# Kernel optimization log

Hardware: AMD Instinct MI355X
Metric: run time of the kernel (lower is better)

Reference implementation:

```python
import jax, jax.numpy as jnp
import numpy as np

B, H, W, C = 4, 128, 128, 256
D_MODEL, NH = 512, 8
DH = D_MODEL // NH  # 64


def setup_inputs() -> dict:
    key = jax.random.key(0)
    ks = jax.random.split(key, 5)
    s = lambda fan_in: 1.0 / np.sqrt(fan_in)
    return {
        "x": jax.random.normal(ks[0], (B, H, W, C), jnp.float32),
        "Wq": jax.random.normal(ks[1], (C, D_MODEL), jnp.float32) * s(C),
        "bq": jnp.zeros((D_MODEL,), jnp.float32),
        "Wk": jax.random.normal(ks[2], (C, D_MODEL), jnp.float32) * s(C),
        "bk": jnp.zeros((D_MODEL,), jnp.float32),
        "Wv": jax.random.normal(ks[3], (C, D_MODEL), jnp.float32) * s(C),
        "bv": jnp.zeros((D_MODEL,), jnp.float32),
        "Wo": jax.random.normal(ks[4], (D_MODEL, C), jnp.float32) * s(D_MODEL),
        "bo": jnp.zeros((C,), jnp.float32),
    }


def reference(x, Wq, bq, Wk, bk, Wv, bv, Wo, bo):
    # Axial multi-head attention along axis 1 (H), W axis is batched.
    b, h, w, _ = x.shape
    q = (x @ Wq + bq).reshape(b, h, w, NH, DH) * (DH ** -0.5)
    k = (x @ Wk + bk).reshape(b, h, w, NH, DH)
    v = (x @ Wv + bv).reshape(b, h, w, NH, DH)
    # scores over the H axis: [B, Nh, W, H, H]
    scores = jnp.einsum("bxwnd,bywnd->bnwxy", q, k)
    probs = jax.nn.softmax(scores, axis=-1)
    # [B, H, W, Nh, DH] -> [B, H, W, d_model]
    out = jnp.einsum("bnwxy,bywnd->bxwnd", probs, v).reshape(b, h, w, D_MODEL)
    # Wo projection; original combines to [B,W,H,C] then permutes back to [B,H,W,C],
    # which is equivalent to applying Wo directly here. Dropout is identity at inference.
    return out @ Wo + bo
```

## Files before the change

### kernel.cpp

```cpp
#include <hip/hip_runtime.h>

typedef unsigned short u16;
typedef __attribute__((ext_vector_type(8))) short bf16x8;
typedef __attribute__((ext_vector_type(8))) unsigned short u16x8;
typedef __attribute__((ext_vector_type(4))) unsigned short u16x4;
typedef __attribute__((ext_vector_type(4))) unsigned u32x4;
typedef __attribute__((ext_vector_type(4))) float f32x4;

#define DEVI static __device__ __forceinline__

DEVI u16 f2b(float f) {
  unsigned u = __builtin_bit_cast(unsigned, f);
  return (u16)((u + 0x7FFFu + ((u >> 16) & 1u)) >> 16);
}

DEVI unsigned cvtpk(float a, float b) {
  unsigned r;
  asm("v_cvt_pk_bf16_f32 %0, %1, %2" : "=v"(r) : "v"(a), "v"(b));
  return r;
}


__global__ __launch_bounds__(256) void prep_x2(const float* __restrict__ x, u16* __restrict__ xb2) {
  const int n8 = 65536 * 256 / 8;
  int i = blockIdx.x * blockDim.x + threadIdx.x;
  for (; i < n8; i += gridDim.x * blockDim.x) {
    const float4* p = (const float4*)x + (size_t)i * 2;
    float4 a = p[0], b = p[1];
    u16x8 r;
    r[0] = f2b(a.x); r[1] = f2b(a.y); r[2] = f2b(a.z); r[3] = f2b(a.w);
    r[4] = f2b(b.x); r[5] = f2b(b.y); r[6] = f2b(b.z); r[7] = f2b(b.w);
    const int t = i >> 5, c0 = (i & 31) * 8;
    const int b_ = t >> 14, y = (t >> 7) & 127, w = t & 127;
    *(u16x8*)(xb2 + (((size_t)(b_ * 128 + w) * 128) + y) * 256 + c0) = r;
  }
}

__global__ __launch_bounds__(256) void prep_w(
    const float* __restrict__ Wq, const float* __restrict__ Wk,
    const float* __restrict__ Wv, const float* __restrict__ Wo,
    const float* __restrict__ bq, const float* __restrict__ bk, const float* __restrict__ bv,
    u16* __restrict__ wqkvT, u16* __restrict__ woT, float* __restrict__ bqkv) {
  const int NW1 = 1536 * 256, NW2 = 256 * 512;
  const int total = NW1 + NW2 + 1536;
  int i = blockIdx.x * blockDim.x + threadIdx.x;
  for (; i < total; i += gridDim.x * blockDim.x) {
    if (i < NW1) {
      int nn = i >> 8, kk = i & 255;
      float v;
      if (nn < 512)       v = Wq[kk * 512 + nn] * 0.125f;
      else if (nn < 1024) v = Wk[kk * 512 + (nn - 512)];
      else                v = Wv[kk * 512 + (nn - 1024)];
      wqkvT[i] = f2b(v);
    } else if (i < NW1 + NW2) {
      int j = i - NW1;
      int nn = j >> 9, kk = j & 511;
      woT[j] = f2b(Wo[kk * 256 + nn]);
    } else {
      int j = i - NW1 - NW2;
      bqkv[j] = (j < 512) ? bq[j] * 0.125f : (j < 1024 ? bk[j - 512] : bv[j - 1024]);
    }
  }
}


__global__ __launch_bounds__(256) void qkv_attn(
    const u16* __restrict__ xb2, const u16* __restrict__ wqkvT,
    const float* __restrict__ bqkv, u16* __restrict__ ao) {
  __shared__ u16 smem[24576];
  u16* qld = smem;
  u16* kld = smem + 8192;
  u16* vt  = smem + 16384;

  const int g = blockIdx.x;
  const int n = g & 7, ct = g >> 3;
  const int tid = threadIdx.x, lane = tid & 63, wid = tid >> 6;
  const int hi = lane >> 4, lo = lane & 15;
  const int wr = wid >> 1, wc = wid & 1;

  const u16* Xp = xb2 + (size_t)ct * 32768;
  const u16* Wq = wqkvT + (size_t)(n * 64 + wc * 32) * 256;
  const u16* Wk = Wq + 512 * 256;
  const u16* Wv = Wq + 1024 * 256;

  bf16x8 areg[4][8];
#pragma unroll
  for (int yT = 0; yT < 4; ++yT)
#pragma unroll
    for (int ks = 0; ks < 8; ++ks)
      areg[yT][ks] = *(const bf16x8*)(Xp + (wr * 64 + yT * 16 + lo) * 256 + hi * 8 + ks * 32);

  {
    f32x4 acc[2][4];
#pragma unroll
    for (int dhT = 0; dhT < 2; ++dhT)
#pragma unroll
      for (int yT = 0; yT < 4; ++yT) acc[dhT][yT] = f32x4{0.f, 0.f, 0.f, 0.f};
#pragma unroll
    for (int ks = 0; ks < 8; ++ks) {
      bf16x8 wf0 = *(const bf16x8*)(Wq + (0 * 16 + lo) * 256 + hi * 8 + ks * 32);
      bf16x8 wf1 = *(const bf16x8*)(Wq + (1 * 16 + lo) * 256 + hi * 8 + ks * 32);
#pragma unroll
      for (int yT = 0; yT < 4; ++yT) {
        acc[0][yT] = __builtin_amdgcn_mfma_f32_16x16x32_bf16(wf0, areg[yT][ks], acc[0][yT], 0, 0, 0);
        acc[1][yT] = __builtin_amdgcn_mfma_f32_16x16x32_bf16(wf1, areg[yT][ks], acc[1][yT], 0, 0, 0);
      }
    }
#pragma unroll
    for (int dhT = 0; dhT < 2; ++dhT) {
      const int dh0 = wc * 32 + dhT * 16 + hi * 4;
      float4 bq4 = *(const float4*)&bqkv[n * 64 + dh0];
#pragma unroll
      for (int yT = 0; yT < 4; ++yT) {
        const int y = wr * 64 + yT * 16 + lo;
        u16x4 pk;
        pk[0] = f2b(acc[dhT][yT][0] + bq4.x);
        pk[1] = f2b(acc[dhT][yT][1] + bq4.y);
        pk[2] = f2b(acc[dhT][yT][2] + bq4.z);
        pk[3] = f2b(acc[dhT][yT][3] + bq4.w);
        *(u16x4*)&qld[y * 64 + (((dh0 >> 3) ^ (y & 7)) << 3) + (dh0 & 7)] = pk;
      }
    }
  }

  {
    f32x4 acc[2][4];
#pragma unroll
    for (int dhT = 0; dhT < 2; ++dhT)
#pragma unroll
      for (int yT = 0; yT < 4; ++yT) acc[dhT][yT] = f32x4{0.f, 0.f, 0.f, 0.f};
#pragma unroll
    for (int ks = 0; ks < 8; ++ks) {
      bf16x8 wf0 = *(const bf16x8*)(Wk + (0 * 16 + lo) * 256 + hi * 8 + ks * 32);
      bf16x8 wf1 = *(const bf16x8*)(Wk + (1 * 16 + lo) * 256 + hi * 8 + ks * 32);
#pragma unroll
      for (int yT = 0; yT < 4; ++yT) {
        acc[0][yT] = __builtin_amdgcn_mfma_f32_16x16x32_bf16(wf0, areg[yT][ks], acc[0][yT], 0, 0, 0);
        acc[1][yT] = __builtin_amdgcn_mfma_f32_16x16x32_bf16(wf1, areg[yT][ks], acc[1][yT], 0, 0, 0);
      }
    }
#pragma unroll
    for (int dhT = 0; dhT < 2; ++dhT) {
      const int dh0 = wc * 32 + dhT * 16 + hi * 4;
#pragma unroll
      for (int yT = 0; yT < 4; ++yT) {
        const int y = wr * 64 + yT * 16 + lo;
        u16x4 pk;
        pk[0] = f2b(acc[dhT][yT][0]);
        pk[1] = f2b(acc[dhT][yT][1]);
        pk[2] = f2b(acc[dhT][yT][2]);
        pk[3] = f2b(acc[dhT][yT][3]);
        *(u16x4*)&kld[y * 64 + (((dh0 >> 3) ^ (y & 7)) << 3) + (dh0 & 7)] = pk;
      }
    }
  }

  {
    f32x4 acc[4][2];
#pragma unroll
    for (int yT = 0; yT < 4; ++yT)
#pragma unroll
      for (int dhT = 0; dhT < 2; ++dhT) acc[yT][dhT] = f32x4{0.f, 0.f, 0.f, 0.f};
#pragma unroll
    for (int ks = 0; ks < 8; ++ks) {
      bf16x8 wf0 = *(const bf16x8*)(Wv + (0 * 16 + lo) * 256 + hi * 8 + ks * 32);
      bf16x8 wf1 = *(const bf16x8*)(Wv + (1 * 16 + lo) * 256 + hi * 8 + ks * 32);
#pragma unroll
      for (int yT = 0; yT < 4; ++yT) {
        acc[yT][0] = __builtin_amdgcn_mfma_f32_16x16x32_bf16(areg[yT][ks], wf0, acc[yT][0], 0, 0, 0);
        acc[yT][1] = __builtin_amdgcn_mfma_f32_16x16x32_bf16(areg[yT][ks], wf1, acc[yT][1], 0, 0, 0);
      }
    }
#pragma unroll
    for (int dhT = 0; dhT < 2; ++dhT) {
      const int dh = wc * 32 + dhT * 16 + lo;
      const float bv = bqkv[1024 + n * 64 + dh];
#pragma unroll
      for (int yT = 0; yT < 4; ++yT) {
        const int y0 = wr * 64 + yT * 16 + hi * 4;
        const int cch = y0 >> 3;
        u16x4 pk;
        pk[0] = f2b(acc[yT][dhT][0] + bv);
        pk[1] = f2b(acc[yT][dhT][1] + bv);
        pk[2] = f2b(acc[yT][dhT][2] + bv);
        pk[3] = f2b(acc[yT][dhT][3] + bv);
        *(u16x4*)&vt[dh * 128 + (((cch & 8) | ((cch & 7) ^ (dh & 7))) << 3) + (y0 & 7)] = pk;
      }
    }
  }

  __syncthreads();

  bf16x8 qf[2][2];
#pragma unroll
  for (int cg = 0; cg < 2; ++cg)
#pragma unroll
    for (int ks = 0; ks < 2; ++ks) {
      const int qr = wid * 32 + cg * 16 + lo;
      qf[cg][ks] = *(const bf16x8*)&qld[qr * 64 + (((hi + ks * 4) ^ (qr & 7)) << 3)];
    }
  f32x4 s2[2][8];
#pragma unroll
  for (int cg = 0; cg < 2; ++cg)
#pragma unroll
    for (int ni = 0; ni < 8; ++ni) s2[cg][ni] = f32x4{0.f, 0.f, 0.f, 0.f};
  __builtin_amdgcn_s_setprio(1);
#pragma unroll
  for (int ks = 0; ks < 2; ++ks)
#pragma unroll
    for (int ni = 0; ni < 8; ++ni) {
      const int kr = ni * 16 + lo;
      bf16x8 kf = *(const bf16x8*)&kld[kr * 64 + (((hi + ks * 4) ^ (kr & 7)) << 3)];
      s2[0][ni] = __builtin_amdgcn_mfma_f32_16x16x32_bf16(kf, qf[0][ks], s2[0][ni], 0, 0, 0);
      s2[1][ni] = __builtin_amdgcn_mfma_f32_16x16x32_bf16(kf, qf[1][ks], s2[1][ni], 0, 0, 0);
    }
  __builtin_amdgcn_s_setprio(0);

  unsigned setA[2][4][2], setB[2][4][2];
#pragma unroll
  for (int cg = 0; cg < 2; ++cg) {
    float mx = s2[cg][0][0];
#pragma unroll
    for (int ni = 0; ni < 8; ++ni)
#pragma unroll
      for (int j = 0; j < 4; ++j) mx = fmaxf(mx, s2[cg][ni][j]);
    mx = fmaxf(mx, __shfl_xor(mx, 16, 64));
    mx = fmaxf(mx, __shfl_xor(mx, 32, 64));
    float sum = 0.f;
#pragma unroll
    for (int ni = 0; ni < 8; ++ni)
#pragma unroll
      for (int j = 0; j < 4; ++j) {
        float e = exp2f((s2[cg][ni][j] - mx) * 1.44269504f);
        s2[cg][ni][j] = e;
        sum += e;
      }
    sum += __shfl_xor(sum, 16, 64);
    sum += __shfl_xor(sum, 32, 64);
    const float r = 1.f / sum;

    unsigned pkE[4][2], pkO[4][2];
#pragma unroll
    for (int o = 0; o < 4; ++o) {
      pkE[o][0] = cvtpk(s2[cg][2 * o][0] * r, s2[cg][2 * o][1] * r);
      pkE[o][1] = cvtpk(s2[cg][2 * o][2] * r, s2[cg][2 * o][3] * r);
      pkO[o][0] = cvtpk(s2[cg][2 * o + 1][0] * r, s2[cg][2 * o + 1][1] * r);
      pkO[o][1] = cvtpk(s2[cg][2 * o + 1][2] * r, s2[cg][2 * o + 1][3] * r);
    }
    const bool lowHi = (hi < 2);
    unsigned keepR[4][2], gotR[4][2];
#pragma unroll
    for (int o = 0; o < 4; ++o)
#pragma unroll
      for (int e = 0; e < 2; ++e) {
        unsigned snd = lowHi ? pkO[o][e] : pkE[o][e];
        keepR[o][e] = lowHi ? pkE[o][e] : pkO[o][e];
        gotR[o][e] = __shfl_xor(snd, 32, 64);
      }
    const bool fwdGot = (hi == 0) || (hi == 3);
    unsigned recv2[4][2];
#pragma unroll
    for (int o = 0; o < 4; ++o)
#pragma unroll
      for (int e = 0; e < 2; ++e) {
        unsigned snd = fwdGot ? gotR[o][e] : keepR[o][e];
        recv2[o][e] = __shfl_xor(snd, 16, 64);
      }
#pragma unroll
    for (int o = 0; o < 4; ++o)
#pragma unroll
      for (int e = 0; e < 2; ++e) {
        setA[cg][o][e] = (hi & 1) ? recv2[o][e] : (hi == 0 ? keepR[o][e] : gotR[o][e]);
        setB[cg][o][e] = (hi & 1) ? (hi == 1 ? gotR[o][e] : keepR[o][e]) : recv2[o][e];
      }
  }

  f32x4 o2[2][4];
#pragma unroll
  for (int cg = 0; cg < 2; ++cg)
#pragma unroll
    for (int ni = 0; ni < 4; ++ni) o2[cg][ni] = f32x4{0.f, 0.f, 0.f, 0.f};
  __builtin_amdgcn_s_setprio(1);
#pragma unroll
  for (int ks = 0; ks < 4; ++ks) {
    const int cch = hi + ks * 4;
    bf16x8 pa[2];
#pragma unroll
    for (int cg = 0; cg < 2; ++cg) {
      u32x4 t;
      t[0] = setA[cg][ks][0]; t[1] = setA[cg][ks][1];
      t[2] = setB[cg][ks][0]; t[3] = setB[cg][ks][1];
      pa[cg] = __builtin_bit_cast(bf16x8, t);
    }
#pragma unroll
    for (int ni = 0; ni < 4; ++ni) {
      const int vr = ni * 16 + lo;
      const int cs = (cch & 8) | ((cch & 7) ^ (vr & 7));
      bf16x8 vf = *(const bf16x8*)&vt[vr * 128 + cs * 8];
      o2[0][ni] = __builtin_amdgcn_mfma_f32_16x16x32_bf16(pa[0], vf, o2[0][ni], 0, 0, 0);
      o2[1][ni] = __builtin_amdgcn_mfma_f32_16x16x32_bf16(pa[1], vf, o2[1][ni], 0, 0, 0);
    }
  }
  __builtin_amdgcn_s_setprio(0);

  const int b_ = ct >> 7, w_ = ct & 127;
#pragma unroll
  for (int cg = 0; cg < 2; ++cg)
#pragma unroll
    for (int j = 0; j < 4; ++j) {
      const int q = wid * 32 + cg * 16 + hi * 4 + j;
      const size_t obase = ((size_t)(b_ * 16384 + q * 128 + w_)) * 512 + (size_t)n * 64;
#pragma unroll
      for (int ni = 0; ni < 4; ++ni)
        ao[obase + ni * 16 + lo] = f2b(o2[cg][ni][j]);
    }
}


DEVI void gload_lds16(const void* g, void* l) {
  __builtin_amdgcn_global_load_lds(
      (const __attribute__((address_space(1))) unsigned int*)g,
      (__attribute__((address_space(3))) unsigned int*)l, 16, 0, 0);
}

template <int KK>
__global__ __launch_bounds__(1024) void gemm256(
    const u16* __restrict__ A, const u16* __restrict__ Bt,
    const float* __restrict__ bias, void* __restrict__ Cv, int N) {
  constexpr int NT = KK / 64;
  __shared__ u16 smem[65536];
  const int tid = threadIdx.x;
  const int lane = tid & 63, wid = tid >> 6;
  const int nTn = N >> 8;
  const int qx = gridDim.x >> 3;
  const int wg = (blockIdx.x & 7) * qx + (blockIdx.x >> 3);
  const long m0 = (long)(wg / nTn) * 256;
  const long n0 = (long)(wg % nTn) * 256;
  const int wr = wid >> 2, wc = wid & 3;
  const int hi = lane >> 4, lo = lane & 15;
  const u16* Ab = A + m0 * KK;
  const u16* Bb = Bt + n0 * KK;
  const int srow_ = tid >> 3;
  const int schunk = tid & 7;

  f32x4 acc[4][4];
#pragma unroll
  for (int mi = 0; mi < 4; ++mi)
#pragma unroll
    for (int ni = 0; ni < 4; ++ni) acc[mi][ni] = f32x4{0.f, 0.f, 0.f, 0.f};

  auto stage = [&](int t) {
    u16* base = &smem[(t & 1) * 32768];
    const int kt = t * 64;
#pragma unroll
    for (int j = 0; j < 2; ++j) {
      int row = j * 128 + srow_;
      int colE = (schunk ^ (row & 7)) << 3;
      gload_lds16(Ab + (long)row * KK + kt + colE, &base[(j * 1024 + tid) * 8]);
    }
#pragma unroll
    for (int j = 0; j < 2; ++j) {
      int row = j * 128 + srow_;
      int colE = (schunk ^ (row & 7)) << 3;
      gload_lds16(Bb + (long)row * KK + kt + colE, &base[16384 + (j * 1024 + tid) * 8]);
    }
  };

  stage(0);
#pragma unroll
  for (int t = 0; t < NT; ++t) {
    if (t + 1 < NT) {
      stage(t + 1);
      asm volatile("s_waitcnt vmcnt(4)" ::: "memory");
    } else {
      asm volatile("s_waitcnt vmcnt(0)" ::: "memory");
    }
    __builtin_amdgcn_sched_barrier(0);
    __builtin_amdgcn_s_barrier();
    const u16* aB = &smem[(t & 1) * 32768];
    const u16* bB = aB + 16384;
#pragma unroll
    for (int ks = 0; ks < 2; ++ks) {
      const int slot = ((hi + ks * 4) ^ (lo & 7)) << 3;
      bf16x8 af[4], bfr[4];
#pragma unroll
      for (int mi = 0; mi < 4; ++mi)
        af[mi] = *(const bf16x8*)&aB[(wr * 64 + mi * 16 + lo) * 64 + slot];
#pragma unroll
      for (int ni = 0; ni < 4; ++ni)
        bfr[ni] = *(const bf16x8*)&bB[(wc * 64 + ni * 16 + lo) * 64 + slot];
#pragma unroll
      for (int mi = 0; mi < 4; ++mi)
#pragma unroll
        for (int ni = 0; ni < 4; ++ni)
          acc[mi][ni] = __builtin_amdgcn_mfma_f32_16x16x32_bf16(af[mi], bfr[ni], acc[mi][ni], 0, 0, 0);
    }
    __builtin_amdgcn_sched_barrier(0);
    __builtin_amdgcn_s_barrier();
  }

  float bb[4];
#pragma unroll
  for (int ni = 0; ni < 4; ++ni) bb[ni] = bias[n0 + wc * 64 + ni * 16 + lo];

  float* Cg = (float*)Cv;
#pragma unroll
  for (int mi = 0; mi < 4; ++mi)
#pragma unroll
    for (int ni = 0; ni < 4; ++ni) {
      long cg = n0 + wc * 64 + ni * 16 + lo;
#pragma unroll
      for (int j = 0; j < 4; ++j)
        Cg[(m0 + wr * 64 + mi * 16 + hi * 4 + j) * N + cg] = acc[mi][ni][j] + bb[ni];
    }
}


extern "C" void kernel_launch(void* const* d_in, const int* in_sizes, int n_in,
                              void* d_out, int out_size, void* d_ws, size_t ws_size,
                              hipStream_t stream) {
  (void)in_sizes; (void)n_in; (void)out_size; (void)ws_size;
  const float* x  = (const float*)d_in[0];
  const float* Wq = (const float*)d_in[1];
  const float* bq = (const float*)d_in[2];
  const float* Wk = (const float*)d_in[3];
  const float* bk = (const float*)d_in[4];
  const float* Wv = (const float*)d_in[5];
  const float* bv = (const float*)d_in[6];
  const float* Wo = (const float*)d_in[7];
  const float* bo = (const float*)d_in[8];
  float* out = (float*)d_out;

  char* ws = (char*)d_ws;
  const size_t MiB = (size_t)1 << 20;
  u16* xb2   = (u16*)(ws + 192 * MiB);
  u16* wqkvT = (u16*)(ws + 224 * MiB);
  u16* woT   = wqkvT + 1536 * 256;
  float* bqkv = (float*)(woT + 256 * 512);

  prep_x2<<<2048, 256, 0, stream>>>(x, xb2);
  prep_w<<<512, 256, 0, stream>>>(Wq, Wk, Wv, Wo, bq, bk, bv, wqkvT, woT, bqkv);

  qkv_attn<<<4096, 256, 0, stream>>>(xb2, wqkvT, bqkv, (u16*)out);
  gemm256<512><<<256, 1024, 0, stream>>>((const u16*)out, woT, bo, out, 256);
}
```

Measured before the change: 223.2 us.

## Stage QKV weights through double-buffered LDS with async global-to-LDS loads

The QKV projection inside the fused attention kernel used to load weight fragments directly from global memory, separately for Q, K and V. It now stages 64-column K-slices of all three weight matrices into a double-buffered, XOR-swizzled LDS region using global_load_lds, with the next slice prefetched while MFMAs run on the current one. The Q, K and V accumulators are computed together in one K loop. This is meant to hide global load latency and share weight traffic across waves. In exchange it adds barriers and keeps more accumulators live, raising register pressure, and it reuses the smem region that later holds q/k/v.

```diff
diff --git a/kernel.cpp b/kernel.cpp
--- a/kernel.cpp
+++ b/kernel.cpp
@@ -18,6 +18,12 @@
   unsigned r;
   asm("v_cvt_pk_bf16_f32 %0, %1, %2" : "=v"(r) : "v"(a), "v"(b));
   return r;
+}
+
+DEVI void gload_lds16(const void* g, void* l) {
+  __builtin_amdgcn_global_load_lds(
+      (const __attribute__((address_space(1))) unsigned int*)g,
+      (__attribute__((address_space(3))) unsigned int*)l, 16, 0, 0);
 }
 
 
@@ -79,9 +85,7 @@
   const int wr = wid >> 1, wc = wid & 1;
 
   const u16* Xp = xb2 + (size_t)ct * 32768;
-  const u16* Wq = wqkvT + (size_t)(n * 64 + wc * 32) * 256;
-  const u16* Wk = Wq + 512 * 256;
-  const u16* Wv = Wq + 1024 * 256;
+  const int hb = n * 64;
 
   bf16x8 areg[4][8];
 #pragma unroll
@@ -90,102 +94,111 @@
     for (int ks = 0; ks < 8; ++ks)
       areg[yT][ks] = *(const bf16x8*)(Xp + (wr * 64 + yT * 16 + lo) * 256 + hi * 8 + ks * 32);
 
-  {
-    f32x4 acc[2][4];
-#pragma unroll
-    for (int dhT = 0; dhT < 2; ++dhT)
-#pragma unroll
-      for (int yT = 0; yT < 4; ++yT) acc[dhT][yT] = f32x4{0.f, 0.f, 0.f, 0.f};
-#pragma unroll
-    for (int ks = 0; ks < 8; ++ks) {
-      bf16x8 wf0 = *(const bf16x8*)(Wq + (0 * 16 + lo) * 256 + hi * 8 + ks * 32);
-      bf16x8 wf1 = *(const bf16x8*)(Wq + (1 * 16 + lo) * 256 + hi * 8 + ks * 32);
-#pragma unroll
-      for (int yT = 0; yT < 4; ++yT) {
-        acc[0][yT] = __builtin_amdgcn_mfma_f32_16x16x32_bf16(wf0, areg[yT][ks], acc[0][yT], 0, 0, 0);
-        acc[1][yT] = __builtin_amdgcn_mfma_f32_16x16x32_bf16(wf1, areg[yT][ks], acc[1][yT], 0, 0, 0);
-      }
-    }
-#pragma unroll
-    for (int dhT = 0; dhT < 2; ++dhT) {
-      const int dh0 = wc * 32 + dhT * 16 + hi * 4;
-      float4 bq4 = *(const float4*)&bqkv[n * 64 + dh0];
-#pragma unroll
-      for (int yT = 0; yT < 4; ++yT) {
-        const int y = wr * 64 + yT * 16 + lo;
-        u16x4 pk;
-        pk[0] = f2b(acc[dhT][yT][0] + bq4.x);
-        pk[1] = f2b(acc[dhT][yT][1] + bq4.y);
-        pk[2] = f2b(acc[dhT][yT][2] + bq4.z);
-        pk[3] = f2b(acc[dhT][yT][3] + bq4.w);
-        *(u16x4*)&qld[y * 64 + (((dh0 >> 3) ^ (y & 7)) << 3) + (dh0 & 7)] = pk;
-      }
-    }
-  }
-
-  {
-    f32x4 acc[2][4];
-#pragma unroll
-    for (int dhT = 0; dhT < 2; ++dhT)
-#pragma unroll
-      for (int yT = 0; yT < 4; ++yT) acc[dhT][yT] = f32x4{0.f, 0.f, 0.f, 0.f};
-#pragma unroll
-    for (int ks = 0; ks < 8; ++ks) {
-      bf16x8 wf0 = *(const bf16x8*)(Wk + (0 * 16 + lo) * 256 + hi * 8 + ks * 32);
-      bf16x8 wf1 = *(const bf16x8*)(Wk + (1 * 16 + lo) * 256 + hi * 8 + ks * 32);
-#pragma unroll
-      for (int yT = 0; yT < 4; ++yT) {
-        acc[0][yT] = __builtin_amdgcn_mfma_f32_16x16x32_bf16(wf0, areg[yT][ks], acc[0][yT], 0, 0, 0);
-        acc[1][yT] = __builtin_amdgcn_mfma_f32_16x16x32_bf16(wf1, areg[yT][ks], acc[1][yT], 0, 0, 0);
-      }
-    }
-#pragma unroll
-    for (int dhT = 0; dhT < 2; ++dhT) {
-      const int dh0 = wc * 32 + dhT * 16 + hi * 4;
-#pragma unroll
-      for (int yT = 0; yT < 4; ++yT) {
-        const int y = wr * 64 + yT * 16 + lo;
-        u16x4 pk;
-        pk[0] = f2b(acc[dhT][yT][0]);
-        pk[1] = f2b(acc[dhT][yT][1]);
-        pk[2] = f2b(acc[dhT][yT][2]);
-        pk[3] = f2b(acc[dhT][yT][3]);
-        *(u16x4*)&kld[y * 64 + (((dh0 >> 3) ^ (y & 7)) << 3) + (dh0 & 7)] = pk;
-      }
-    }
-  }
-
-  {
-    f32x4 acc[4][2];
-#pragma unroll
-    for (int yT = 0; yT < 4; ++yT)
-#pragma unroll
-      for (int dhT = 0; dhT < 2; ++dhT) acc[yT][dhT] = f32x4{0.f, 0.f, 0.f, 0.f};
-#pragma unroll
-    for (int ks = 0; ks < 8; ++ks) {
-      bf16x8 wf0 = *(const bf16x8*)(Wv + (0 * 16 + lo) * 256 + hi * 8 + ks * 32);
-      bf16x8 wf1 = *(const bf16x8*)(Wv + (1 * 16 + lo) * 256 + hi * 8 + ks * 32);
-#pragma unroll
-      for (int yT = 0; yT < 4; ++yT) {
-        acc[yT][0] = __builtin_amdgcn_mfma_f32_16x16x32_bf16(areg[yT][ks], wf0, acc[yT][0], 0, 0, 0);
-        acc[yT][1] = __builtin_amdgcn_mfma_f32_16x16x32_bf16(areg[yT][ks], wf1, acc[yT][1], 0, 0, 0);
-      }
-    }
-#pragma unroll
-    for (int dhT = 0; dhT < 2; ++dhT) {
-      const int dh = wc * 32 + dhT * 16 + lo;
-      const float bv = bqkv[1024 + n * 64 + dh];
-#pragma unroll
-      for (int yT = 0; yT < 4; ++yT) {
-        const int y0 = wr * 64 + yT * 16 + hi * 4;
-        const int cch = y0 >> 3;
-        u16x4 pk;
-        pk[0] = f2b(acc[yT][dhT][0] + bv);
-        pk[1] = f2b(acc[yT][dhT][1] + bv);
-        pk[2] = f2b(acc[yT][dhT][2] + bv);
-        pk[3] = f2b(acc[yT][dhT][3] + bv);
-        *(u16x4*)&vt[dh * 128 + (((cch & 8) | ((cch & 7) ^ (dh & 7))) << 3) + (y0 & 7)] = pk;
-      }
+  auto stageW = [&](int kt) {
+    u16* dst = &smem[(kt & 1) * 12288];
+    const int kc = kt * 64;
+#pragma unroll
+    for (int it = 0; it < 6; ++it) {
+      const int c = it * 256 + tid;
+      const int sr = c >> 3, ch = c & 7;
+      const int grow = hb + ((sr >> 6) << 9) + (sr & 63);
+      const int gcol = kc + ((ch ^ (sr & 7)) << 3);
+      gload_lds16(wqkvT + (size_t)grow * 256 + gcol, &dst[c * 8]);
+    }
+  };
+
+  f32x4 aq[2][4], ak[2][4], av[4][2];
+#pragma unroll
+  for (int i2 = 0; i2 < 2; ++i2)
+#pragma unroll
+    for (int j4 = 0; j4 < 4; ++j4) {
+      aq[i2][j4] = f32x4{0.f, 0.f, 0.f, 0.f};
+      ak[i2][j4] = f32x4{0.f, 0.f, 0.f, 0.f};
+      av[j4][i2] = f32x4{0.f, 0.f, 0.f, 0.f};
+    }
+
+  stageW(0);
+#pragma unroll
+  for (int kt = 0; kt < 4; ++kt) {
+    if (kt < 3) {
+      stageW(kt + 1);
+      asm volatile("s_waitcnt vmcnt(6)" ::: "memory");
+    } else {
+      asm volatile("s_waitcnt vmcnt(0)" ::: "memory");
+    }
+    __builtin_amdgcn_sched_barrier(0);
+    __builtin_amdgcn_s_barrier();
+    const u16* wb = &smem[(kt & 1) * 12288];
+#pragma unroll
+    for (int ks2 = 0; ks2 < 2; ++ks2) {
+      const int cs = ((hi + ks2 * 4) ^ (lo & 7)) << 3;
+      {
+        bf16x8 w0 = *(const bf16x8*)&wb[(wc * 32 + lo) * 64 + cs];
+        bf16x8 w1 = *(const bf16x8*)&wb[(wc * 32 + 16 + lo) * 64 + cs];
+#pragma unroll
+        for (int yT = 0; yT < 4; ++yT) {
+          aq[0][yT] = __builtin_amdgcn_mfma_f32_16x16x32_bf16(w0, areg[yT][2 * kt + ks2], aq[0][yT], 0, 0, 0);
+          aq[1][yT] = __builtin_amdgcn_mfma_f32_16x16x32_bf16(w1, areg[yT][2 * kt + ks2], aq[1][yT], 0, 0, 0);
+        }
+      }
+      {
+        bf16x8 w0 = *(const bf16x8*)&wb[(64 + wc * 32 + lo) * 64 + cs];
+        bf16x8 w1 = *(const bf16x8*)&wb[(64 + wc * 32 + 16 + lo) * 64 + cs];
+#pragma unroll
+        for (int yT = 0; yT < 4; ++yT) {
+          ak[0][yT] = __builtin_amdgcn_mfma_f32_16x16x32_bf16(w0, areg[yT][2 * kt + ks2], ak[0][yT], 0, 0, 0);
+          ak[1][yT] = __builtin_amdgcn_mfma_f32_16x16x32_bf16(w1, areg[yT][2 * kt + ks2], ak[1][yT], 0, 0, 0);
+        }
+      }
+      {
+        bf16x8 w0 = *(const bf16x8*)&wb[(128 + wc * 32 + lo) * 64 + cs];
+        bf16x8 w1 = *(const bf16x8*)&wb[(128 + wc * 32 + 16 + lo) * 64 + cs];
+#pragma unroll
+        for (int yT = 0; yT < 4; ++yT) {
+          av[yT][0] = __builtin_amdgcn_mfma_f32_16x16x32_bf16(areg[yT][2 * kt + ks2], w0, av[yT][0], 0, 0, 0);
+          av[yT][1] = __builtin_amdgcn_mfma_f32_16x16x32_bf16(areg[yT][2 * kt + ks2], w1, av[yT][1], 0, 0, 0);
+        }
+      }
+    }
+    __builtin_amdgcn_sched_barrier(0);
+    __builtin_amdgcn_s_barrier();
+  }
+
+#pragma unroll
+  for (int dhT = 0; dhT < 2; ++dhT) {
+    const int dh0 = wc * 32 + dhT * 16 + hi * 4;
+    float4 bq4 = *(const float4*)&bqkv[n * 64 + dh0];
+#pragma unroll
+    for (int yT = 0; yT < 4; ++yT) {
+      const int y = wr * 64 + yT * 16 + lo;
+      u16x4 pkq;
+      pkq[0] = f2b(aq[dhT][yT][0] + bq4.x);
+      pkq[1] = f2b(aq[dhT][yT][1] + bq4.y);
+      pkq[2] = f2b(aq[dhT][yT][2] + bq4.z);
+      pkq[3] = f2b(aq[dhT][yT][3] + bq4.w);
+      *(u16x4*)&qld[y * 64 + (((dh0 >> 3) ^ (y & 7)) << 3) + (dh0 & 7)] = pkq;
+      u16x4 pkk;
+      pkk[0] = f2b(ak[dhT][yT][0]);
+      pkk[1] = f2b(ak[dhT][yT][1]);
+      pkk[2] = f2b(ak[dhT][yT][2]);
+      pkk[3] = f2b(ak[dhT][yT][3]);
+      *(u16x4*)&kld[y * 64 + (((dh0 >> 3) ^ (y & 7)) << 3) + (dh0 & 7)] = pkk;
+    }
+  }
+#pragma unroll
+  for (int dhT = 0; dhT < 2; ++dhT) {
+    const int dh = wc * 32 + dhT * 16 + lo;
+    const float bv = bqkv[1024 + n * 64 + dh];
+#pragma unroll
+    for (int yT = 0; yT < 4; ++yT) {
+      const int y0 = wr * 64 + yT * 16 + hi * 4;
+      const int cch = y0 >> 3;
+      u16x4 pk;
+      pk[0] = f2b(av[yT][dhT][0] + bv);
+      pk[1] = f2b(av[yT][dhT][1] + bv);
+      pk[2] = f2b(av[yT][dhT][2] + bv);
+      pk[3] = f2b(av[yT][dhT][3] + bv);
+      *(u16x4*)&vt[dh * 128 + (((cch & 8) | ((cch & 7) ^ (dh & 7))) << 3) + (y0 & 7)] = pk;
     }
   }
 
@@ -316,12 +329,6 @@
     }
 }
 
-
-DEVI void gload_lds16(const void* g, void* l) {
-  __builtin_amdgcn_global_load_lds(
-      (const __attribute__((address_space(1))) unsigned int*)g,
-      (__attribute__((address_space(3))) unsigned int*)l, 16, 0, 0);
-}
 
 template <int KK>
 __global__ __launch_bounds__(1024) void gemm256(
```

After: 230.3 us. 3.2% more time.
